# Kernel optimization log

Measured on AMD Instinct MI355X. Metric: run time of the kernel, lower is better.

## Reference

```python
import jax, jax.numpy as jnp
import numpy as np

N_FFT = 1024
HOP = 512


def _overlap_add_50pct(frames):
    """Stateful 50% overlap-add. frames: (B, N, n_fft) -> (B, N, hop).
    Each frame is split into (curr, next); output[t] = curr[t] + next[t-1]."""
    xs = jnp.moveaxis(frames, 1, 0)  # (N, B, n_fft) for scan over frames

    def step(carry, x):
        x_curr = x[..., :HOP]
        x_next = x[..., HOP:]
        return x_next, x_curr + carry

    init = jnp.zeros((xs.shape[1], HOP), dtype=frames.dtype)
    _, ys = jax.lax.scan(step, init, xs)  # ys: (N, B, hop)
    return jnp.moveaxis(ys, 0, 1)  # (B, N, hop)


def _istft(re, im):
    spec = jax.lax.complex(re, im)               # (B, N, n_fft//2+1)
    frames = jnp.fft.irfft(spec, n=N_FFT, axis=-1)  # (B, N, n_fft), real IFFT
    frames = frames * jnp.asarray(0.5, frames.dtype)  # MulHalf (window_fn=None path)
    return _overlap_add_50pct(frames)            # (B, N, hop)


def setup_inputs() -> dict:
    key = jax.random.key(0)
    k1, k2 = jax.random.split(key)
    B, N = 8, 4000
    re = jax.random.normal(k1, (B, N, N_FFT // 2 + 1), dtype=jnp.float32)
    im = jax.random.normal(k2, (B, N, N_FFT // 2 + 1), dtype=jnp.float32)
    return {"re": re, "im": im}


def reference(re, im):
    return _istft(re, im)
```

## Files before the change

kernel.cpp:

```cpp
#include <hip/hip_runtime.h>
#include <math.h>

#define NBINS 513
#define NROWS 4000
#define BATCH 8
#define FPW   8
#define CHAINS_PER_BATCH (NROWS / FPW)

__device__ __forceinline__ void cmul(float& ar, float& ai, float br, float bi) {
    const float t = ar * br - ai * bi;
    ai = ar * bi + ai * br;
    ar = t;
}

__device__ __forceinline__ void idft8(float* xr, float* xi) {
    const float S = 0.70710678118654752440f;
    float er[4], ei[4], orr[4], oi[4];
    #pragma unroll
    for (int j = 0; j < 4; ++j) {
        er[j]  = xr[j] + xr[j+4];  ei[j] = xi[j] + xi[j+4];
        orr[j] = xr[j] - xr[j+4];  oi[j] = xi[j] - xi[j+4];
    }
    const float f1r = S * (orr[1] - oi[1]), f1i = S * (orr[1] + oi[1]);
    const float f2r = -oi[2],               f2i = orr[2];
    const float f3r = S * (-orr[3] - oi[3]), f3i = S * (orr[3] - oi[3]);
    {
        const float eer = er[0]+er[2], eei = ei[0]+ei[2];
        const float eor = er[0]-er[2], eoi = ei[0]-ei[2];
        const float oer = er[1]+er[3], oei = ei[1]+ei[3];
        const float oor = er[1]-er[3], ooi = ei[1]-ei[3];
        xr[0] = eer + oer;  xi[0] = eei + oei;
        xr[2] = eor - ooi;  xi[2] = eoi + oor;
        xr[4] = eer - oer;  xi[4] = eei - oei;
        xr[6] = eor + ooi;  xi[6] = eoi - oor;
    }
    {
        const float eer = orr[0]+f2r, eei = oi[0]+f2i;
        const float eor = orr[0]-f2r, eoi = oi[0]-f2i;
        const float oer = f1r+f3r,    oei = f1i+f3i;
        const float oor = f1r-f3r,    ooi = f1i-f3i;
        xr[1] = eer + oer;  xi[1] = eei + oei;
        xr[3] = eor - ooi;  xi[3] = eoi + oor;
        xr[5] = eer - oer;  xi[5] = eei - oei;
        xr[7] = eor + ooi;  xi[7] = eoi - oor;
    }
}

__global__ __launch_bounds__(64) void istft_kernel(
    const float* __restrict__ re, const float* __restrict__ im,
    float* __restrict__ out)
{
    __shared__ float2 ex2[512];

    const int u  = threadIdx.x;
    const int b  = blockIdx.y;
    const int t0 = blockIdx.x * FPW;

    const int k1 = u >> 3;
    const int k2 = u & 7;

    const float w0 = 6.283185307179586476925f / 1024.0f;
    float2 twp[8];
    #pragma unroll
    for (int j = 0; j < 8; ++j) {
        float s, c; sincosf(w0 * (float)(u + 64 * j), &s, &c);
        twp[j] = make_float2(c, s);
    }
    float2 wA, wB0, wBs;
    {
        float s, c;
        sincosf(w0 * (float)(16 * k1), &s, &c);     wA  = make_float2(c, s);
        sincosf(w0 * (float)(2 * k2 * k1), &s, &c); wB0 = make_float2(c, s);
        sincosf(w0 * (float)(16 * k2), &s, &c);     wBs = make_float2(c, s);
    }

    float2 cc[4];
    #pragma unroll
    for (int m = 0; m < 4; ++m) cc[m] = make_float2(0.f, 0.f);

    float pxr[8], pxi[8], pmr[8], pmi[8];

    auto issue_loads = [&](int t) {
        if (t >= 0) {
            const size_t base = ((size_t)b * NROWS + (size_t)t) * NBINS;
            const float* rp = re + base;
            const float* ip = im + base;
            #pragma unroll
            for (int j = 0; j < 8; ++j) {
                const int k = u + 64 * j;
                pxr[j] = rp[k];        pxi[j] = ip[k];
                pmr[j] = rp[512 - k];  pmi[j] = ip[512 - k];
            }
        } else {
            #pragma unroll
            for (int j = 0; j < 8; ++j) { pxr[j]=0.f; pxi[j]=0.f; pmr[j]=0.f; pmi[j]=0.f; }
        }
    };

    issue_loads(t0 - 1);

    for (int t = t0 - 1; t < t0 + FPW; ++t) {
        float zr8[8], zi8[8];
        {
            const float F = 4.8828125e-4f;
            #pragma unroll
            for (int j = 0; j < 8; ++j) {
                const int k = u + 64 * j;
                float xr = pxr[j], xi = pxi[j];
                float rc = pmr[j], ic = -pmi[j];
                if (k == 0) { xi = 0.f; ic = 0.f; }
                const float er = F * (xr + rc), ei = F * (xi + ic);
                const float hr = F * (xr - rc), hi = F * (xi - ic);
                const float o_r = twp[j].x * hr - twp[j].y * hi;
                const float o_i = twp[j].x * hi + twp[j].y * hr;
                zr8[j] = er - o_i;
                zi8[j] = ei + o_r;
            }
        }

        if (t + 1 < t0 + FPW) issue_loads(t + 1);

        idft8(zr8, zi8);
        {
            float tr = wA.x, ti = wA.y;
            #pragma unroll
            for (int m0 = 1; m0 < 8; ++m0) {
                cmul(zr8[m0], zi8[m0], tr, ti);
                cmul(tr, ti, wA.x, wA.y);
            }
        }
        #pragma unroll
        for (int m0 = 0; m0 < 8; ++m0)
            ex2[64 * m0 + 8 * ((k1 ^ m0) & 7) + k2] = make_float2(zr8[m0], zi8[m0]);
        #pragma unroll
        for (int kk = 0; kk < 8; ++kk) {
            const float2 v = ex2[64 * k1 + 8 * ((kk ^ k1) & 7) + k2];
            zr8[kk] = v.x; zi8[kk] = v.y;
        }

        idft8(zr8, zi8);
        {
            float tr = wB0.x, ti = wB0.y;
            #pragma unroll
            for (int m1 = 0; m1 < 8; ++m1) {
                cmul(zr8[m1], zi8[m1], tr, ti);
                cmul(tr, ti, wBs.x, wBs.y);
            }
        }
        #pragma unroll
        for (int m1 = 0; m1 < 8; ++m1)
            ex2[64 * k2 + 8 * ((m1 ^ k2) & 7) + k1] = make_float2(zr8[m1], zi8[m1]);
        #pragma unroll
        for (int kk = 0; kk < 8; ++kk) {
            const float2 v = ex2[64 * kk + 8 * ((k1 ^ kk) & 7) + k2];
            zr8[kk] = v.x; zi8[kk] = v.y;
        }

        idft8(zr8, zi8);

        if (t >= t0) {
            float2* orow = (float2*)(out + ((size_t)b * NROWS + (size_t)t) * 512);
            #pragma unroll
            for (int m = 0; m < 4; ++m)
                orow[u + 64 * m] = make_float2(zr8[m] + cc[m].x, zi8[m] + cc[m].y);
        }
        #pragma unroll
        for (int m = 0; m < 4; ++m) cc[m] = make_float2(zr8[m + 4], zi8[m + 4]);
    }
}

extern "C" void kernel_launch(void* const* d_in, const int* in_sizes, int n_in,
                              void* d_out, int out_size, void* d_ws, size_t ws_size,
                              hipStream_t stream) {
    const float* re = (const float*)d_in[0];
    const float* im = (const float*)d_in[1];
    float* out = (float*)d_out;
    dim3 grid(CHAINS_PER_BATCH, BATCH);
    istft_kernel<<<grid, 64, 0, stream>>>(re, im, out);
}
```

Measured before the change: 46.32 us.

## Process two interleaved frame chains per wavefront with float4 LDS exchange

Each 64-thread block now runs two independent 8-frame chains together, interleaving their FFT math for more instruction-level parallelism. The two chains share twiddle computation and swap data through float4 LDS accesses instead of float2. The 1/2048 scale is folded into the precomputed twiddles, and the grid is halved. Register pressure roughly doubles, which may lower occupancy, and there are fewer blocks to hide memory latency.

```diff
diff --git a/kernel.cpp b/kernel.cpp
--- a/kernel.cpp
+++ b/kernel.cpp
@@ -50,21 +50,24 @@
     const float* __restrict__ re, const float* __restrict__ im,
     float* __restrict__ out)
 {
-    __shared__ float2 ex2[512];
-
-    const int u  = threadIdx.x;
-    const int b  = blockIdx.y;
-    const int t0 = blockIdx.x * FPW;
+    __shared__ float4 ex4[512];
+
+    const int u   = threadIdx.x;
+    const int b   = blockIdx.y;
+    const int t0A = (blockIdx.x * 2)     * FPW;
+    const int t0B = (blockIdx.x * 2 + 1) * FPW;
 
     const int k1 = u >> 3;
     const int k2 = u & 7;
 
     const float w0 = 6.283185307179586476925f / 1024.0f;
-    float2 twp[8];
+    const float F  = 4.8828125e-4f;
+
+    float2 twn[8];
     #pragma unroll
     for (int j = 0; j < 8; ++j) {
         float s, c; sincosf(w0 * (float)(u + 64 * j), &s, &c);
-        twp[j] = make_float2(c, s);
+        twn[j] = make_float2(-F * s, F * c);
     }
     float2 wA, wB0, wBs;
     {
@@ -74,98 +77,121 @@
         sincosf(w0 * (float)(16 * k2), &s, &c);     wBs = make_float2(c, s);
     }
 
-    float2 cc[4];
+    float2 cc[2][4];
     #pragma unroll
-    for (int m = 0; m < 4; ++m) cc[m] = make_float2(0.f, 0.f);
-
-    float pxr[8], pxi[8], pmr[8], pmi[8];
-
-    auto issue_loads = [&](int t) {
-        if (t >= 0) {
-            const size_t base = ((size_t)b * NROWS + (size_t)t) * NBINS;
-            const float* rp = re + base;
-            const float* ip = im + base;
+    for (int q = 0; q < 2; ++q)
+        #pragma unroll
+        for (int m = 0; m < 4; ++m) cc[q][m] = make_float2(0.f, 0.f);
+
+    const float* rebase = re + (size_t)b * NROWS * NBINS;
+    const float* imbase = im + (size_t)b * NROWS * NBINS;
+
+    float pxr[2][8], pxi[2][8], pmr[2][8], pmi[2][8];
+
+    auto issue_loads = [&](int it) {
+        #pragma unroll
+        for (int q = 0; q < 2; ++q) {
+            const int t = (q ? t0B : t0A) - 1 + it;
+            if (t >= 0) {
+                const float* rp = rebase + (size_t)t * NBINS;
+                const float* ip = imbase + (size_t)t * NBINS;
+                #pragma unroll
+                for (int j = 0; j < 8; ++j) {
+                    const int k = u + 64 * j;
+                    pxr[q][j] = rp[k];        pxi[q][j] = ip[k];
+                    pmr[q][j] = rp[512 - k];  pmi[q][j] = ip[512 - k];
+                }
+            } else {
+                #pragma unroll
+                for (int j = 0; j < 8; ++j) {
+                    pxr[q][j]=0.f; pxi[q][j]=0.f; pmr[q][j]=0.f; pmi[q][j]=0.f;
+                }
+            }
+        }
+    };
+
+    issue_loads(0);
+
+    for (int it = 0; it <= FPW; ++it) {
+        float zr[2][8], zi[2][8];
+        #pragma unroll
+        for (int q = 0; q < 2; ++q) {
             #pragma unroll
             for (int j = 0; j < 8; ++j) {
                 const int k = u + 64 * j;
-                pxr[j] = rp[k];        pxi[j] = ip[k];
-                pmr[j] = rp[512 - k];  pmi[j] = ip[512 - k];
-            }
-        } else {
-            #pragma unroll
-            for (int j = 0; j < 8; ++j) { pxr[j]=0.f; pxi[j]=0.f; pmr[j]=0.f; pmi[j]=0.f; }
-        }
-    };
-
-    issue_loads(t0 - 1);
-
-    for (int t = t0 - 1; t < t0 + FPW; ++t) {
-        float zr8[8], zi8[8];
-        {
-            const float F = 4.8828125e-4f;
-            #pragma unroll
-            for (int j = 0; j < 8; ++j) {
-                const int k = u + 64 * j;
-                float xr = pxr[j], xi = pxi[j];
-                float rc = pmr[j], ic = -pmi[j];
+                float xr = pxr[q][j], xi = pxi[q][j];
+                float rc = pmr[q][j], ic = -pmi[q][j];
                 if (k == 0) { xi = 0.f; ic = 0.f; }
-                const float er = F * (xr + rc), ei = F * (xi + ic);
-                const float hr = F * (xr - rc), hi = F * (xi - ic);
-                const float o_r = twp[j].x * hr - twp[j].y * hi;
-                const float o_i = twp[j].x * hi + twp[j].y * hr;
-                zr8[j] = er - o_i;
-                zi8[j] = ei + o_r;
-            }
-        }
-
-        if (t + 1 < t0 + FPW) issue_loads(t + 1);
-
-        idft8(zr8, zi8);
+                const float er0 = xr + rc, ei0 = xi + ic;
+                const float hr0 = xr - rc, hi0 = xi - ic;
+                zr[q][j] = F * er0 + (twn[j].x * hr0 - twn[j].y * hi0);
+                zi[q][j] = F * ei0 + (twn[j].x * hi0 + twn[j].y * hr0);
+            }
+        }
+
+        if (it < FPW) issue_loads(it + 1);
+
+        idft8(zr[0], zi[0]);
+        idft8(zr[1], zi[1]);
         {
             float tr = wA.x, ti = wA.y;
             #pragma unroll
             for (int m0 = 1; m0 < 8; ++m0) {
-                cmul(zr8[m0], zi8[m0], tr, ti);
+                cmul(zr[0][m0], zi[0][m0], tr, ti);
+                cmul(zr[1][m0], zi[1][m0], tr, ti);
                 cmul(tr, ti, wA.x, wA.y);
             }
         }
         #pragma unroll
         for (int m0 = 0; m0 < 8; ++m0)
-            ex2[64 * m0 + 8 * ((k1 ^ m0) & 7) + k2] = make_float2(zr8[m0], zi8[m0]);
+            ex4[64 * m0 + 8 * ((k1 ^ m0) & 7) + k2] =
+                make_float4(zr[0][m0], zi[0][m0], zr[1][m0], zi[1][m0]);
         #pragma unroll
         for (int kk = 0; kk < 8; ++kk) {
-            const float2 v = ex2[64 * k1 + 8 * ((kk ^ k1) & 7) + k2];
-            zr8[kk] = v.x; zi8[kk] = v.y;
-        }
-
-        idft8(zr8, zi8);
+            const float4 v = ex4[64 * k1 + 8 * ((kk ^ k1) & 7) + k2];
+            zr[0][kk] = v.x; zi[0][kk] = v.y; zr[1][kk] = v.z; zi[1][kk] = v.w;
+        }
+
+        idft8(zr[0], zi[0]);
+        idft8(zr[1], zi[1]);
         {
             float tr = wB0.x, ti = wB0.y;
             #pragma unroll
             for (int m1 = 0; m1 < 8; ++m1) {
-                cmul(zr8[m1], zi8[m1], tr, ti);
+                cmul(zr[0][m1], zi[0][m1], tr, ti);
+                cmul(zr[1][m1], zi[1][m1], tr, ti);
                 cmul(tr, ti, wBs.x, wBs.y);
             }
         }
         #pragma unroll
         for (int m1 = 0; m1 < 8; ++m1)
-            ex2[64 * k2 + 8 * ((m1 ^ k2) & 7) + k1] = make_float2(zr8[m1], zi8[m1]);
+            ex4[64 * k2 + 8 * ((m1 ^ k2) & 7) + k1] =
+                make_float4(zr[0][m1], zi[0][m1], zr[1][m1], zi[1][m1]);
         #pragma unroll
         for (int kk = 0; kk < 8; ++kk) {
-            const float2 v = ex2[64 * kk + 8 * ((k1 ^ kk) & 7) + k2];
-            zr8[kk] = v.x; zi8[kk] = v.y;
-        }
-
-        idft8(zr8, zi8);
-
-        if (t >= t0) {
-            float2* orow = (float2*)(out + ((size_t)b * NROWS + (size_t)t) * 512);
+            const float4 v = ex4[64 * kk + 8 * ((k1 ^ kk) & 7) + k2];
+            zr[0][kk] = v.x; zi[0][kk] = v.y; zr[1][kk] = v.z; zi[1][kk] = v.w;
+        }
+
+        idft8(zr[0], zi[0]);
+        idft8(zr[1], zi[1]);
+
+        if (it >= 1) {
+            #pragma unroll
+            for (int q = 0; q < 2; ++q) {
+                const int t = (q ? t0B : t0A) - 1 + it;
+                float2* orow = (float2*)(out + ((size_t)b * NROWS + (size_t)t) * 512);
+                #pragma unroll
+                for (int m = 0; m < 4; ++m)
+                    orow[u + 64 * m] =
+                        make_float2(zr[q][m] + cc[q][m].x, zi[q][m] + cc[q][m].y);
+            }
+        }
+        #pragma unroll
+        for (int q = 0; q < 2; ++q)
             #pragma unroll
             for (int m = 0; m < 4; ++m)
-                orow[u + 64 * m] = make_float2(zr8[m] + cc[m].x, zi8[m] + cc[m].y);
-        }
-        #pragma unroll
-        for (int m = 0; m < 4; ++m) cc[m] = make_float2(zr8[m + 4], zi8[m + 4]);
+                cc[q][m] = make_float2(zr[q][m + 4], zi[q][m + 4]);
     }
 }
 
@@ -175,6 +201,6 @@
     const float* re = (const float*)d_in[0];
     const float* im = (const float*)d_in[1];
     float* out = (float*)d_out;
-    dim3 grid(CHAINS_PER_BATCH, BATCH);
+    dim3 grid(CHAINS_PER_BATCH / 2, BATCH);
     istft_kernel<<<grid, 64, 0, stream>>>(re, im, out);
 }
```

Measured after the change: 66.01 us. +42.5%, slower.

## Stage spectrum rows into LDS with async global_load_lds double buffering

Applied to the files above, without the earlier changes.

Replaces the per-thread register prefetch of each frame's re/im bins with direct global-to-LDS loads (`global_load_lds`) into a double-buffered shared staging area. The next frame is fetched while the current one is transformed. Each bin is now fetched from global memory once, and the mirrored bin (512-k) is read from LDS instead of being loaded a second time. The 1/N scale is also folded into the precomputed twiddles to save multiplies. In exchange it adds LDS traffic and relies on hand-tuned `s_waitcnt vmcnt` counts that must match the number of loads and stores in flight. If those counts are off, a stage could be read before its loads finish.

```diff
diff --git a/kernel.cpp b/kernel.cpp
--- a/kernel.cpp
+++ b/kernel.cpp
@@ -6,6 +6,9 @@
 #define BATCH 8
 #define FPW   8
 #define CHAINS_PER_BATCH (NROWS / FPW)
+
+typedef const __attribute__((address_space(1))) void* gvp;
+typedef __attribute__((address_space(3))) void* lvp;
 
 __device__ __forceinline__ void cmul(float& ar, float& ai, float br, float bi) {
     const float t = ar * br - ai * bi;
@@ -50,6 +53,7 @@
     const float* __restrict__ re, const float* __restrict__ im,
     float* __restrict__ out)
 {
+    __shared__ float  st[2][2][516];
     __shared__ float2 ex2[512];
 
     const int u  = threadIdx.x;
@@ -60,11 +64,13 @@
     const int k2 = u & 7;
 
     const float w0 = 6.283185307179586476925f / 1024.0f;
-    float2 twp[8];
+    const float F  = 4.8828125e-4f;
+
+    float2 twn[8];
     #pragma unroll
     for (int j = 0; j < 8; ++j) {
         float s, c; sincosf(w0 * (float)(u + 64 * j), &s, &c);
-        twp[j] = make_float2(c, s);
+        twn[j] = make_float2(-F * s, F * c);
     }
     float2 wA, wB0, wBs;
     {
@@ -78,47 +84,60 @@
     #pragma unroll
     for (int m = 0; m < 4; ++m) cc[m] = make_float2(0.f, 0.f);
 
-    float pxr[8], pxi[8], pmr[8], pmi[8];
+    const float* rebase = re + (size_t)b * NROWS * NBINS;
+    const float* imbase = im + (size_t)b * NROWS * NBINS;
 
-    auto issue_loads = [&](int t) {
-        if (t >= 0) {
-            const size_t base = ((size_t)b * NROWS + (size_t)t) * NBINS;
-            const float* rp = re + base;
-            const float* ip = im + base;
+    auto stage = [&](int t, int buf) {
+        const float* rp = rebase + (size_t)t * NBINS;
+        const float* ip = imbase + (size_t)t * NBINS;
+        #pragma unroll
+        for (int jj = 0; jj < 8; ++jj)
+            __builtin_amdgcn_global_load_lds((gvp)(rp + 64 * jj + u),
+                                             (lvp)&st[buf][0][64 * jj], 4, 0, 0);
+        __builtin_amdgcn_global_load_lds((gvp)(rp + 449 + u),
+                                         (lvp)&st[buf][0][449], 4, 0, 0);
+        #pragma unroll
+        for (int jj = 0; jj < 8; ++jj)
+            __builtin_amdgcn_global_load_lds((gvp)(ip + 64 * jj + u),
+                                             (lvp)&st[buf][1][64 * jj], 4, 0, 0);
+        __builtin_amdgcn_global_load_lds((gvp)(ip + 449 + u),
+                                         (lvp)&st[buf][1][449], 4, 0, 0);
+    };
+
+    if (t0 == 0) {
+        #pragma unroll
+        for (int j = 0; j < 8; ++j) { st[0][0][u + 64 * j] = 0.f; st[0][1][u + 64 * j] = 0.f; }
+        if (u == 0) { st[0][0][512] = 0.f; st[0][1][512] = 0.f; }
+    } else {
+        stage(t0 - 1, 0);
+    }
+    asm volatile("s_waitcnt vmcnt(0)" ::: "memory");
+
+    for (int it = 0; it <= FPW; ++it) {
+        const int t = t0 - 1 + it;
+        const int c = it & 1;
+
+        if (it >= 2)      { asm volatile("s_waitcnt vmcnt(8)" ::: "memory"); }
+        else if (it == 1) { asm volatile("s_waitcnt vmcnt(0)" ::: "memory"); }
+
+        float zr8[8], zi8[8];
+        {
+            const float* fr = st[c][0];
+            const float* fi = st[c][1];
             #pragma unroll
             for (int j = 0; j < 8; ++j) {
                 const int k = u + 64 * j;
-                pxr[j] = rp[k];        pxi[j] = ip[k];
-                pmr[j] = rp[512 - k];  pmi[j] = ip[512 - k];
-            }
-        } else {
-            #pragma unroll
-            for (int j = 0; j < 8; ++j) { pxr[j]=0.f; pxi[j]=0.f; pmr[j]=0.f; pmi[j]=0.f; }
-        }
-    };
-
-    issue_loads(t0 - 1);
-
-    for (int t = t0 - 1; t < t0 + FPW; ++t) {
-        float zr8[8], zi8[8];
-        {
-            const float F = 4.8828125e-4f;
-            #pragma unroll
-            for (int j = 0; j < 8; ++j) {
-                const int k = u + 64 * j;
-                float xr = pxr[j], xi = pxi[j];
-                float rc = pmr[j], ic = -pmi[j];
+                float xr = fr[k], xi = fi[k];
+                float rc = fr[512 - k], ic = -fi[512 - k];
                 if (k == 0) { xi = 0.f; ic = 0.f; }
-                const float er = F * (xr + rc), ei = F * (xi + ic);
-                const float hr = F * (xr - rc), hi = F * (xi - ic);
-                const float o_r = twp[j].x * hr - twp[j].y * hi;
-                const float o_i = twp[j].x * hi + twp[j].y * hr;
-                zr8[j] = er - o_i;
-                zi8[j] = ei + o_r;
+                const float er0 = xr + rc, ei0 = xi + ic;
+                const float hr0 = xr - rc, hi0 = xi - ic;
+                zr8[j] = F * er0 + (twn[j].x * hr0 - twn[j].y * hi0);
+                zi8[j] = F * ei0 + (twn[j].x * hi0 + twn[j].y * hr0);
             }
         }
 
-        if (t + 1 < t0 + FPW) issue_loads(t + 1);
+        if (it < FPW) stage(t + 1, c ^ 1);
 
         idft8(zr8, zi8);
         {
@@ -158,7 +177,7 @@
 
         idft8(zr8, zi8);
 
-        if (t >= t0) {
+        if (it >= 1) {
             float2* orow = (float2*)(out + ((size_t)b * NROWS + (size_t)t) * 512);
             #pragma unroll
             for (int m = 0; m < 4; ++m)
```

Measured after the change: 43.76 us. 5.5% less time.
